# Kernel tuning notes

Hardware: AMD Instinct MI355X
Metric: run time of the kernel (lower is better)

The kernel has to match this reference:

```python
import jax, jax.numpy as jnp
import numpy as np

N = 100000        # nodes in the batched graph
E = 1_600_000     # directed edges
G = 256           # graphs in the batch
IN, H = 3, 64
EPS = 1e-5        # BatchNorm eps (eval mode: running stats, dropout off)


def setup_inputs() -> dict:
    key = jax.random.key(0)
    ks = jax.random.split(key, 40)
    inp = {}
    inp["x"] = jax.random.normal(ks[0], (N, IN), jnp.float32)
    inp["edge_index"] = jax.random.randint(ks[1], (2, E), 0, N, dtype=jnp.int32)
    inp["batch_idx"] = jnp.sort(jax.random.randint(ks[2], (N,), 0, G, dtype=jnp.int32))
    dims = [IN, H, H, H]  # zip(dims[:-1], dims[1:]) -> 3 GCN layers (as in source)
    k = 3
    for i in range(3):
        inp[f"W{i}"] = jax.random.normal(ks[k], (dims[i], dims[i + 1]), jnp.float32) * 0.1; k += 1
        inp[f"b{i}"] = jax.random.normal(ks[k], (dims[i + 1],), jnp.float32) * 0.01; k += 1
        inp[f"g{i}"] = jax.random.uniform(ks[k], (dims[i + 1],), jnp.float32, 0.5, 1.5); k += 1
        inp[f"be{i}"] = jax.random.normal(ks[k], (dims[i + 1],), jnp.float32) * 0.1; k += 1
        inp[f"rm{i}"] = jax.random.normal(ks[k], (dims[i + 1],), jnp.float32) * 0.1; k += 1
        inp[f"rv{i}"] = jax.random.uniform(ks[k], (dims[i + 1],), jnp.float32, 0.5, 1.5); k += 1
    inp["mW1"] = jax.random.normal(ks[k], (2 * H, 32), jnp.float32) * 0.1; k += 1
    inp["mb1"] = jnp.zeros((32,), jnp.float32)
    inp["mW2"] = jax.random.normal(ks[k], (32, 16), jnp.float32) * 0.1; k += 1
    inp["mb2"] = jnp.zeros((16,), jnp.float32)
    inp["mW3"] = jax.random.normal(ks[k], (16, 1), jnp.float32) * 0.1; k += 1
    inp["mb3"] = jnp.zeros((1,), jnp.float32)
    return inp


def _gcn(x, W, b, src, dst):
    # PyG GCNConv: add self-loops, symmetric D^-1/2 (A+I) D^-1/2 normalization
    h = x @ W                                   # [N, out]
    deg = jnp.zeros((N,), h.dtype).at[dst].add(1.0) + 1.0  # +1 self-loop
    dinv = jax.lax.rsqrt(deg)
    coef = dinv[src] * dinv[dst]                # [E]
    agg = jax.ops.segment_sum(h[src] * coef[:, None], dst, num_segments=N)
    agg = agg + h * (dinv * dinv)[:, None]      # self-loop message
    return agg + b


def _bn(x, g, be, rm, rv):
    return (x - rm) * jax.lax.rsqrt(rv + EPS) * g + be


def _forward(x, edge_index, batch_idx,
             W0, b0, g0, be0, rm0, rv0,
             W1, b1, g1, be1, rm1, rv1,
             W2, b2, g2, be2, rm2, rv2,
             mW1, mb1, mW2, mb2, mW3, mb3):
    src, dst = edge_index[0], edge_index[1]
    layers = [(W0, b0, g0, be0, rm0, rv0), (W1, b1, g1, be1, rm1, rv1), (W2, b2, g2, be2, rm2, rv2)]
    for (W, b, g, be, rm, rv) in layers:
        x = jax.nn.relu(_bn(_gcn(x, W, b, src, dst), g, be, rm, rv))
    cnt = jax.ops.segment_sum(jnp.ones((N,), x.dtype), batch_idx, num_segments=G)
    x_mean = jax.ops.segment_sum(x, batch_idx, num_segments=G) / jnp.maximum(cnt, 1.0)[:, None]
    x_max = jax.ops.segment_max(x, batch_idx, num_segments=G)
    x_max = jnp.where(jnp.isfinite(x_max), x_max, 0.0)
    xg = jnp.concatenate([x_mean, x_max], axis=1)  # [G, 2H]
    h = jax.nn.relu(xg @ mW1 + mb1)
    h = jax.nn.relu(h @ mW2 + mb2)
    return h @ mW3 + mb3                            # [G, 1]


def reference(x, edge_index, batch_idx,
              W0, b0, g0, be0, rm0, rv0,
              W1, b1, g1, be1, rm1, rv1,
              W2, b2, g2, be2, rm2, rv2,
              mW1, mb1, mW2, mb2, mW3, mb3):
    return _forward(x, edge_index, batch_idx,
                    W0, b0, g0, be0, rm0, rv0,
                    W1, b1, g1, be1, rm1, rv1,
                    W2, b2, g2, be2, rm2, rv2,
                    mW1, mb1, mW2, mb2, mW3, mb3)
```

## Files before the change

### kernel.cpp

```cpp
#include <hip/hip_runtime.h>
#include <hip/hip_fp16.h>

#define NN 100000
#define EE 1600000
#define GG 256
#define EPS 1e-5f
#define KB2 ((NN + 511) >> 9)
#define EPB 4096
#define EBLK ((EE + EPB - 1) / EPB)
#define NB256 ((NN + 255) / 256)

__device__ __forceinline__ unsigned int pack2(float x, float y) {
  __half2 h = __float22half2_rn(make_float2(x, y));
  return *reinterpret_cast<unsigned int*>(&h);
}
__device__ __forceinline__ uint2 pack4(float x, float y, float z, float w) {
  uint2 r;
  r.x = pack2(x, y);
  r.y = pack2(z, w);
  return r;
}
__device__ __forceinline__ void add8(float4& a0, float4& a1, uint4 v) {
  __half2 h0 = *reinterpret_cast<__half2*>(&v.x);
  __half2 h1 = *reinterpret_cast<__half2*>(&v.y);
  __half2 h2 = *reinterpret_cast<__half2*>(&v.z);
  __half2 h3 = *reinterpret_cast<__half2*>(&v.w);
  float2 f0 = __half22float2(h0), f1 = __half22float2(h1);
  float2 f2 = __half22float2(h2), f3 = __half22float2(h3);
  a0.x += f0.x; a0.y += f0.y; a0.z += f1.x; a0.w += f1.y;
  a1.x += f2.x; a1.y += f2.y; a1.z += f3.x; a1.w += f3.y;
}

__global__ void k_bcnt(const int* __restrict__ ei, int* __restrict__ bcnt) {
  __shared__ int cnt[KB2];
  int t = threadIdx.x;
  for (int i = t; i < KB2; i += 256) cnt[i] = 0;
  __syncthreads();
  int e0 = blockIdx.x * EPB;
#pragma unroll
  for (int j = 0; j < 16; ++j) {
    int e = e0 + j * 256 + t;
    if (e < EE) atomicAdd(&cnt[ei[EE + e] >> 9], 1);
  }
  __syncthreads();
  for (int i = t; i < KB2; i += 256)
    if (cnt[i] > 0) atomicAdd(&bcnt[i], cnt[i]);
}

__global__ void k_bscan(const int* __restrict__ bcnt, int* __restrict__ bbase,
                        int* __restrict__ bfill, int* __restrict__ row) {
  __shared__ int s[256];
  int t = threadIdx.x;
  int v = (t < KB2) ? bcnt[t] : 0;
  s[t] = v;
  __syncthreads();
  for (int off = 1; off < 256; off <<= 1) {
    int add = (t >= off) ? s[t - off] : 0;
    __syncthreads();
    s[t] += add;
    __syncthreads();
  }
  if (t < KB2) {
    int e = s[t] - v;
    bbase[t] = e;
    bfill[t] = e;
  }
  if (t == 0) {
    bbase[KB2] = EE;
    row[NN] = EE;
  }
}

__global__ void k_passA(const int* __restrict__ ei, int* __restrict__ bfill,
                        int* __restrict__ tmp) {
  __shared__ int cnt[KB2], cur[KB2], base[KB2];
  int t = threadIdx.x;
  for (int b = t; b < KB2; b += 256) { cnt[b] = 0; cur[b] = 0; }
  __syncthreads();
  int e0 = blockIdx.x * EPB;
  int myb[16];
#pragma unroll
  for (int j = 0; j < 16; ++j) {
    int e = e0 + j * 256 + t;
    int bb = -1;
    if (e < EE) bb = ei[EE + e] >> 9;
    myb[j] = bb;
    if (bb >= 0) atomicAdd(&cnt[bb], 1);
  }
  __syncthreads();
  for (int b = t; b < KB2; b += 256)
    if (cnt[b] > 0) base[b] = atomicAdd(&bfill[b], cnt[b]);
  __syncthreads();
#pragma unroll
  for (int j = 0; j < 16; ++j) {
    int e = e0 + j * 256 + t;
    int bb = myb[j];
    if (bb >= 0) {
      int slot = base[bb] + atomicAdd(&cur[bb], 1);
      tmp[slot] = (ei[e] << 9) | (ei[EE + e] & 511);
    }
  }
}

__global__ void k_bucket(const int* __restrict__ tmp, const int* __restrict__ bbase,
                         const float* __restrict__ x, int* __restrict__ csr,
                         int* __restrict__ row, float* __restrict__ dinv,
                         float4* __restrict__ xd) {
  __shared__ int cnt[512], s[512], fillp[512];
  int b = blockIdx.x, t = threadIdx.x;
  int nb = b << 9;
  int e0 = bbase[b], e1 = bbase[b + 1];
  cnt[t] = 0;
  cnt[t + 256] = 0;
  __syncthreads();
  for (int e = e0 + t; e < e1; e += 256) atomicAdd(&cnt[tmp[e] & 511], 1);
  __syncthreads();
  s[t] = cnt[t];
  s[t + 256] = cnt[t + 256];
  __syncthreads();
  for (int off = 1; off < 512; off <<= 1) {
    int i1 = t + 256;
    int v0 = (t >= off) ? s[t - off] : 0;
    int v1 = (i1 >= off) ? s[i1 - off] : 0;
    __syncthreads();
    s[t] += v0;
    s[i1] += v1;
    __syncthreads();
  }
#pragma unroll
  for (int k = 0; k < 2; ++k) {
    int i = t + k * 256;
    int excl = s[i] - cnt[i];
    fillp[i] = excl;
    int dst = nb + i;
    if (dst < NN) {
      row[dst] = e0 + excl;
      float d = rsqrtf((float)cnt[i] + 1.0f);
      dinv[dst] = d;
      xd[dst] = make_float4(x[dst * 3] * d, x[dst * 3 + 1] * d, x[dst * 3 + 2] * d, 0.f);
    }
  }
  __syncthreads();
  for (int e = e0 + t; e < e1; e += 256) {
    int ed = tmp[e];
    int slot = atomicAdd(&fillp[ed & 511], 1);
    csr[e0 + slot] = ed >> 9;
  }
}

__global__ void k_agg3f(const float4* __restrict__ xd, const int* __restrict__ row,
                        const int* __restrict__ csr, const float* __restrict__ dinv,
                        const float* __restrict__ W, const float* __restrict__ b,
                        const float* __restrict__ gam, const float* __restrict__ bet,
                        const float* __restrict__ rm, const float* __restrict__ rv,
                        uint2* __restrict__ out) {
  int n = blockIdx.x * 256 + threadIdx.x;
  if (n >= NN) return;
  int s0 = row[n], s1 = row[n + 1];
  float4 a = xd[n];
  float ax = a.x, ay = a.y, az = a.z;
  for (int i = s0; i < s1; i += 16) {
    int rem = s1 - i;
    int idx[16];
#pragma unroll
    for (int j = 0; j < 16; ++j) idx[j] = csr[min(i + j, s1 - 1)];
    float4 v[16];
#pragma unroll
    for (int j = 0; j < 16; ++j) v[j] = xd[idx[j]];
#pragma unroll
    for (int j = 0; j < 16; ++j)
      if (j < rem) { ax += v[j].x; ay += v[j].y; az += v[j].z; }
  }
  float d = dinv[n];
  float t0 = ax * d, t1 = ay * d, t2 = az * d;
  const float4* W4 = (const float4*)W;
  const float4* b4 = (const float4*)b;
  const float4* g4p = (const float4*)gam;
  const float4* be4p = (const float4*)bet;
  const float4* rm4p = (const float4*)rm;
  const float4* rv4p = (const float4*)rv;
#pragma unroll
  for (int c4 = 0; c4 < 16; ++c4) {
    float4 w0 = W4[c4], w1 = W4[16 + c4], w2 = W4[32 + c4];
    float4 bb = b4[c4], g4 = g4p[c4], be4 = be4p[c4], rm4 = rm4p[c4], rv4 = rv4p[c4];
    float4 o;
    o.x = fmaf(t0, w0.x, fmaf(t1, w1.x, fmaf(t2, w2.x, bb.x)));
    o.y = fmaf(t0, w0.y, fmaf(t1, w1.y, fmaf(t2, w2.y, bb.y)));
    o.z = fmaf(t0, w0.z, fmaf(t1, w1.z, fmaf(t2, w2.z, bb.z)));
    o.w = fmaf(t0, w0.w, fmaf(t1, w1.w, fmaf(t2, w2.w, bb.w)));
    float scx = g4.x * rsqrtf(rv4.x + EPS), shx = be4.x - rm4.x * scx;
    float scy = g4.y * rsqrtf(rv4.y + EPS), shy = be4.y - rm4.y * scy;
    float scz = g4.z * rsqrtf(rv4.z + EPS), shz = be4.z - rm4.z * scz;
    float scw = g4.w * rsqrtf(rv4.w + EPS), shw = be4.w - rm4.w * scw;
    o.x = fmaxf(fmaf(o.x, scx, shx), 0.f) * d;
    o.y = fmaxf(fmaf(o.y, scy, shy), 0.f) * d;
    o.z = fmaxf(fmaf(o.z, scz, shz), 0.f) * d;
    o.w = fmaxf(fmaf(o.w, scw, shw), 0.f) * d;
    out[(size_t)n * 16 + c4] = pack4(o.x, o.y, o.z, o.w);
  }
}

template <bool MID>
__global__ void k_layer2(const uint4* __restrict__ xs, const int* __restrict__ row,
                         const int* __restrict__ csr, const float* __restrict__ dinv,
                         const float* __restrict__ W, const float* __restrict__ b,
                         const float* __restrict__ gam, const float* __restrict__ bet,
                         const float* __restrict__ rm, const float* __restrict__ rv,
                         void* __restrict__ outv) {
  __shared__ float sh[32][68];
  int t = blockIdx.x * 256 + threadIdx.x;
  int n = t >> 3, sub = t & 7;
  int local = threadIdx.x >> 3;
  int s0 = row[n], s1 = row[n + 1];
  float4 a0 = make_float4(0.f, 0.f, 0.f, 0.f);
  float4 a1 = make_float4(0.f, 0.f, 0.f, 0.f);
  add8(a0, a1, xs[(size_t)n * 8 + sub]);
  if (s0 < s1) {
    int e = s0 + sub;
    int myidx = (e < s1) ? csr[e] : n;
    for (int i = s0; i < s1; i += 8) {
      int e2 = i + 8 + sub;
      int pre = csr[min(e2, s1 - 1)];
      int nidx = (e2 < s1) ? pre : n;
      int rem = s1 - i;
      uint4 v[8];
#pragma unroll
      for (int j = 0; j < 8; ++j) {
        int idx = __shfl(myidx, j, 8);
        v[j] = xs[(size_t)idx * 8 + sub];
      }
#pragma unroll
      for (int j = 0; j < 8; ++j)
        if (j < rem) add8(a0, a1, v[j]);
      myidx = nidx;
    }
  }
  float d = dinv[n];
  float4 w0 = make_float4(a0.x * d, a0.y * d, a0.z * d, a0.w * d);
  float4 w1 = make_float4(a1.x * d, a1.y * d, a1.z * d, a1.w * d);
  *(float4*)&sh[local][sub * 8] = w0;
  *(float4*)&sh[local][sub * 8 + 4] = w1;
  __syncthreads();
  const float4* W4 = (const float4*)W;
  float4 accA = ((const float4*)b)[sub * 2];
  float4 accB = ((const float4*)b)[sub * 2 + 1];
#pragma unroll 8
  for (int k = 0; k < 64; ++k) {
    float xv = sh[local][k];
    float4 wA = W4[k * 16 + sub * 2];
    float4 wB = W4[k * 16 + sub * 2 + 1];
    accA.x = fmaf(xv, wA.x, accA.x);
    accA.y = fmaf(xv, wA.y, accA.y);
    accA.z = fmaf(xv, wA.z, accA.z);
    accA.w = fmaf(xv, wA.w, accA.w);
    accB.x = fmaf(xv, wB.x, accB.x);
    accB.y = fmaf(xv, wB.y, accB.y);
    accB.z = fmaf(xv, wB.z, accB.z);
    accB.w = fmaf(xv, wB.w, accB.w);
  }
  float4 gA = ((const float4*)gam)[sub * 2], gB = ((const float4*)gam)[sub * 2 + 1];
  float4 beA = ((const float4*)bet)[sub * 2], beB = ((const float4*)bet)[sub * 2 + 1];
  float4 rmA = ((const float4*)rm)[sub * 2], rmB = ((const float4*)rm)[sub * 2 + 1];
  float4 rvA = ((const float4*)rv)[sub * 2], rvB = ((const float4*)rv)[sub * 2 + 1];
  float4 oA, oB;
  {
    float sc = gA.x * rsqrtf(rvA.x + EPS); oA.x = fmaxf(fmaf(accA.x, sc, beA.x - rmA.x * sc), 0.f);
    sc = gA.y * rsqrtf(rvA.y + EPS); oA.y = fmaxf(fmaf(accA.y, sc, beA.y - rmA.y * sc), 0.f);
    sc = gA.z * rsqrtf(rvA.z + EPS); oA.z = fmaxf(fmaf(accA.z, sc, beA.z - rmA.z * sc), 0.f);
    sc = gA.w * rsqrtf(rvA.w + EPS); oA.w = fmaxf(fmaf(accA.w, sc, beA.w - rmA.w * sc), 0.f);
    sc = gB.x * rsqrtf(rvB.x + EPS); oB.x = fmaxf(fmaf(accB.x, sc, beB.x - rmB.x * sc), 0.f);
    sc = gB.y * rsqrtf(rvB.y + EPS); oB.y = fmaxf(fmaf(accB.y, sc, beB.y - rmB.y * sc), 0.f);
    sc = gB.z * rsqrtf(rvB.z + EPS); oB.z = fmaxf(fmaf(accB.z, sc, beB.z - rmB.z * sc), 0.f);
    sc = gB.w * rsqrtf(rvB.w + EPS); oB.w = fmaxf(fmaf(accB.w, sc, beB.w - rmB.w * sc), 0.f);
  }
  if (MID) {
    uint4 r;
    r.x = pack2(oA.x * d, oA.y * d);
    r.y = pack2(oA.z * d, oA.w * d);
    r.z = pack2(oB.x * d, oB.y * d);
    r.w = pack2(oB.z * d, oB.w * d);
    ((uint4*)outv)[(size_t)n * 8 + sub] = r;
  } else {
    ((float4*)outv)[(size_t)n * 16 + sub * 2] = oA;
    ((float4*)outv)[(size_t)n * 16 + sub * 2 + 1] = oB;
  }
}

__device__ __forceinline__ int lower_bound(const int* __restrict__ b, int target) {
  int lo = 0, hi = NN;
  while (lo < hi) {
    int m = (lo + hi) >> 1;
    if (b[m] < target) lo = m + 1; else hi = m;
  }
  return lo;
}

__global__ void k_poolmlp(const float4* __restrict__ feat, const int* __restrict__ bidx,
                          const float* __restrict__ mW1, const float* __restrict__ mb1,
                          const float* __restrict__ mW2, const float* __restrict__ mb2,
                          const float* __restrict__ mW3, const float* __restrict__ mb3,
                          float* __restrict__ out) {
  __shared__ float4 shs[16][17], shm[16][17];
  __shared__ float xg[128], h1[32], h2[16];
  int g = blockIdx.x, t = threadIdx.x;
  int c4 = t & 15, r = t >> 4;
  int lo = lower_bound(bidx, g);
  int hi = lower_bound(bidx, g + 1);
  float4 s = make_float4(0.f, 0.f, 0.f, 0.f);
  float4 m = make_float4(0.f, 0.f, 0.f, 0.f);
  for (int i = lo + r; i < hi; i += 16) {
    float4 v = feat[(size_t)i * 16 + c4];
    s.x += v.x; s.y += v.y; s.z += v.z; s.w += v.w;
    m.x = fmaxf(m.x, v.x); m.y = fmaxf(m.y, v.y);
    m.z = fmaxf(m.z, v.z); m.w = fmaxf(m.w, v.w);
  }
  shs[r][c4] = s;
  shm[r][c4] = m;
  __syncthreads();
  if (t < 16) {
    float4 cs = shs[0][t], cm = shm[0][t];
#pragma unroll
    for (int r2 = 1; r2 < 16; ++r2) {
      float4 as = shs[r2][t], am = shm[r2][t];
      cs.x += as.x; cs.y += as.y; cs.z += as.z; cs.w += as.w;
      cm.x = fmaxf(cm.x, am.x); cm.y = fmaxf(cm.y, am.y);
      cm.z = fmaxf(cm.z, am.z); cm.w = fmaxf(cm.w, am.w);
    }
    float inv = 1.0f / fmaxf((float)(hi - lo), 1.0f);
    xg[t * 4 + 0] = cs.x * inv; xg[t * 4 + 1] = cs.y * inv;
    xg[t * 4 + 2] = cs.z * inv; xg[t * 4 + 3] = cs.w * inv;
    xg[64 + t * 4 + 0] = cm.x; xg[64 + t * 4 + 1] = cm.y;
    xg[64 + t * 4 + 2] = cm.z; xg[64 + t * 4 + 3] = cm.w;
  }
  __syncthreads();
  if (t < 32) {
    float a = mb1[t];
    for (int k = 0; k < 128; ++k) a = fmaf(xg[k], mW1[k * 32 + t], a);
    h1[t] = fmaxf(a, 0.f);
  }
  __syncthreads();
  if (t < 16) {
    float a = mb2[t];
    for (int k = 0; k < 32; ++k) a = fmaf(h1[k], mW2[k * 16 + t], a);
    h2[t] = fmaxf(a, 0.f);
  }
  __syncthreads();
  if (t == 0) {
    float a = mb3[0];
    for (int k = 0; k < 16; ++k) a = fmaf(h2[k], mW3[k], a);
    out[g] = a;
  }
}

extern "C" void kernel_launch(void* const* d_in, const int* in_sizes, int n_in,
                              void* d_out, int out_size, void* d_ws, size_t ws_size,
                              hipStream_t stream) {
  const float* x = (const float*)d_in[0];
  const int* ei = (const int*)d_in[1];
  const int* bidx = (const int*)d_in[2];
  const float *W[3], *b[3], *gam[3], *bet[3], *rm[3], *rv[3];
  for (int l = 0; l < 3; ++l) {
    W[l] = (const float*)d_in[3 + 6 * l];
    b[l] = (const float*)d_in[4 + 6 * l];
    gam[l] = (const float*)d_in[5 + 6 * l];
    bet[l] = (const float*)d_in[6 + 6 * l];
    rm[l] = (const float*)d_in[7 + 6 * l];
    rv[l] = (const float*)d_in[8 + 6 * l];
  }
  const float* mW1 = (const float*)d_in[21];
  const float* mb1 = (const float*)d_in[22];
  const float* mW2 = (const float*)d_in[23];
  const float* mb2 = (const float*)d_in[24];
  const float* mW3 = (const float*)d_in[25];
  const float* mb3 = (const float*)d_in[26];
  float* out = (float*)d_out;

  char* ws = (char*)d_ws;
  size_t off = 0;
  auto alloc = [&](size_t bytes) {
    void* p = ws + off;
    off = (off + bytes + 1023) & ~(size_t)1023;
    return p;
  };
  float* dinv = (float*)alloc(NN * 4);
  int* row = (int*)alloc((NN + 1) * 4);
  int* csr = (int*)alloc((size_t)EE * 4);
  int* bcnt = (int*)alloc(256 * 4);
  int* bbase = (int*)alloc(256 * 4);
  int* bfill = (int*)alloc(256 * 4);
  float4* xd = (float4*)alloc((size_t)NN * 16);
  float* bufA = (float*)alloc((size_t)NN * 64 * 4);
  float* bufB = (float*)alloc((size_t)NN * 64 * 4);
  int* tmp = (int*)bufA;

  hipMemsetAsync(bcnt, 0, 256 * 4, stream);

  k_bcnt<<<EBLK, 256, 0, stream>>>(ei, bcnt);
  k_bscan<<<1, 256, 0, stream>>>(bcnt, bbase, bfill, row);
  k_passA<<<EBLK, 256, 0, stream>>>(ei, bfill, tmp);
  k_bucket<<<KB2, 256, 0, stream>>>(tmp, bbase, x, csr, row, dinv, xd);

  int nb8 = (NN * 8) / 256;

  k_agg3f<<<NB256, 256, 0, stream>>>(xd, row, csr, dinv, W[0], b[0], gam[0], bet[0],
                                     rm[0], rv[0], (uint2*)bufA);
  k_layer2<true><<<nb8, 256, 0, stream>>>((const uint4*)bufA, row, csr, dinv, W[1], b[1],
                                          gam[1], bet[1], rm[1], rv[1], (void*)bufB);
  k_layer2<false><<<nb8, 256, 0, stream>>>((const uint4*)bufB, row, csr, dinv, W[2], b[2],
                                           gam[2], bet[2], rm[2], rv[2], (void*)bufA);
  k_poolmlp<<<GG, 256, 0, stream>>>((const float4*)bufA, bidx, mW1, mb1, mW2, mb2, mW3, mb3, out);
}
```

Measured before the change: 343.9 us.

## Replace bucket count/scan with fixed-capacity buckets and asm-batched gathers

```diff
diff --git a/kernel.cpp b/kernel.cpp
--- a/kernel.cpp
+++ b/kernel.cpp
@@ -6,6 +6,7 @@
 #define GG 256
 #define EPS 1e-5f
 #define KB2 ((NN + 511) >> 9)
+#define BCAP 10240
 #define EPB 4096
 #define EBLK ((EE + EPB - 1) / EPB)
 #define NB256 ((NN + 255) / 256)
@@ -31,44 +32,11 @@
   a1.x += f2.x; a1.y += f2.y; a1.z += f3.x; a1.w += f3.y;
 }
 
-__global__ void k_bcnt(const int* __restrict__ ei, int* __restrict__ bcnt) {
-  __shared__ int cnt[KB2];
-  int t = threadIdx.x;
-  for (int i = t; i < KB2; i += 256) cnt[i] = 0;
-  __syncthreads();
-  int e0 = blockIdx.x * EPB;
-#pragma unroll
-  for (int j = 0; j < 16; ++j) {
-    int e = e0 + j * 256 + t;
-    if (e < EE) atomicAdd(&cnt[ei[EE + e] >> 9], 1);
-  }
-  __syncthreads();
-  for (int i = t; i < KB2; i += 256)
-    if (cnt[i] > 0) atomicAdd(&bcnt[i], cnt[i]);
-}
-
-__global__ void k_bscan(const int* __restrict__ bcnt, int* __restrict__ bbase,
-                        int* __restrict__ bfill, int* __restrict__ row) {
-  __shared__ int s[256];
-  int t = threadIdx.x;
-  int v = (t < KB2) ? bcnt[t] : 0;
-  s[t] = v;
-  __syncthreads();
-  for (int off = 1; off < 256; off <<= 1) {
-    int add = (t >= off) ? s[t - off] : 0;
-    __syncthreads();
-    s[t] += add;
-    __syncthreads();
-  }
-  if (t < KB2) {
-    int e = s[t] - v;
-    bbase[t] = e;
-    bfill[t] = e;
-  }
-  if (t == 0) {
-    bbase[KB2] = EE;
-    row[NN] = EE;
-  }
+__device__ __forceinline__ void gld16(uint4& d, const uint4* p) {
+  asm volatile("global_load_dwordx4 %0, %1, off" : "=v"(d) : "v"(p));
+}
+__device__ __forceinline__ void gld4(int& d, const int* p) {
+  asm volatile("global_load_dword %0, %1, off" : "=v"(d) : "v"(p));
 }
 
 __global__ void k_passA(const int* __restrict__ ei, int* __restrict__ bfill,
@@ -89,7 +57,7 @@
   }
   __syncthreads();
   for (int b = t; b < KB2; b += 256)
-    if (cnt[b] > 0) base[b] = atomicAdd(&bfill[b], cnt[b]);
+    if (cnt[b] > 0) base[b] = b * BCAP + atomicAdd(&bfill[b], cnt[b]);
   __syncthreads();
 #pragma unroll
   for (int j = 0; j < 16; ++j) {
@@ -102,14 +70,14 @@
   }
 }
 
-__global__ void k_bucket(const int* __restrict__ tmp, const int* __restrict__ bbase,
+__global__ void k_bucket(const int* __restrict__ tmp, const int* __restrict__ bfill,
                          const float* __restrict__ x, int* __restrict__ csr,
-                         int* __restrict__ row, float* __restrict__ dinv,
-                         float4* __restrict__ xd) {
+                         int* __restrict__ row, int* __restrict__ rowe,
+                         float* __restrict__ dinv, float4* __restrict__ xd) {
   __shared__ int cnt[512], s[512], fillp[512];
   int b = blockIdx.x, t = threadIdx.x;
   int nb = b << 9;
-  int e0 = bbase[b], e1 = bbase[b + 1];
+  int e0 = b * BCAP, e1 = e0 + bfill[b];
   cnt[t] = 0;
   cnt[t + 256] = 0;
   __syncthreads();
@@ -135,6 +103,7 @@
     int dst = nb + i;
     if (dst < NN) {
       row[dst] = e0 + excl;
+      rowe[dst] = e0 + s[i];
       float d = rsqrtf((float)cnt[i] + 1.0f);
       dinv[dst] = d;
       xd[dst] = make_float4(x[dst * 3] * d, x[dst * 3 + 1] * d, x[dst * 3 + 2] * d, 0.f);
@@ -149,14 +118,15 @@
 }
 
 __global__ void k_agg3f(const float4* __restrict__ xd, const int* __restrict__ row,
-                        const int* __restrict__ csr, const float* __restrict__ dinv,
+                        const int* __restrict__ rowe, const int* __restrict__ csr,
+                        const float* __restrict__ dinv,
                         const float* __restrict__ W, const float* __restrict__ b,
                         const float* __restrict__ gam, const float* __restrict__ bet,
                         const float* __restrict__ rm, const float* __restrict__ rv,
                         uint2* __restrict__ out) {
   int n = blockIdx.x * 256 + threadIdx.x;
   if (n >= NN) return;
-  int s0 = row[n], s1 = row[n + 1];
+  int s0 = row[n], s1 = rowe[n];
   float4 a = xd[n];
   float ax = a.x, ay = a.y, az = a.z;
   for (int i = s0; i < s1; i += 16) {
@@ -201,8 +171,10 @@
 }
 
 template <bool MID>
+__launch_bounds__(256, 4)
 __global__ void k_layer2(const uint4* __restrict__ xs, const int* __restrict__ row,
-                         const int* __restrict__ csr, const float* __restrict__ dinv,
+                         const int* __restrict__ rowe, const int* __restrict__ csr,
+                         const float* __restrict__ dinv,
                          const float* __restrict__ W, const float* __restrict__ b,
                          const float* __restrict__ gam, const float* __restrict__ bet,
                          const float* __restrict__ rm, const float* __restrict__ rv,
@@ -211,7 +183,7 @@
   int t = blockIdx.x * 256 + threadIdx.x;
   int n = t >> 3, sub = t & 7;
   int local = threadIdx.x >> 3;
-  int s0 = row[n], s1 = row[n + 1];
+  int s0 = row[n], s1 = rowe[n];
   float4 a0 = make_float4(0.f, 0.f, 0.f, 0.f);
   float4 a1 = make_float4(0.f, 0.f, 0.f, 0.f);
   add8(a0, a1, xs[(size_t)n * 8 + sub]);
@@ -220,19 +192,29 @@
     int myidx = (e < s1) ? csr[e] : n;
     for (int i = s0; i < s1; i += 8) {
       int e2 = i + 8 + sub;
-      int pre = csr[min(e2, s1 - 1)];
-      int nidx = (e2 < s1) ? pre : n;
+      int pre;
+      gld4(pre, csr + min(e2, s1 - 1));
+      uint4 v0, v1, v2, v3, v4, v5, v6, v7;
+      gld16(v0, xs + ((size_t)__shfl(myidx, 0, 8) * 8 + sub));
+      gld16(v1, xs + ((size_t)__shfl(myidx, 1, 8) * 8 + sub));
+      gld16(v2, xs + ((size_t)__shfl(myidx, 2, 8) * 8 + sub));
+      gld16(v3, xs + ((size_t)__shfl(myidx, 3, 8) * 8 + sub));
+      gld16(v4, xs + ((size_t)__shfl(myidx, 4, 8) * 8 + sub));
+      gld16(v5, xs + ((size_t)__shfl(myidx, 5, 8) * 8 + sub));
+      gld16(v6, xs + ((size_t)__shfl(myidx, 6, 8) * 8 + sub));
+      gld16(v7, xs + ((size_t)__shfl(myidx, 7, 8) * 8 + sub));
+      asm volatile("s_waitcnt vmcnt(0)" ::: "memory");
+      __builtin_amdgcn_sched_barrier(0);
       int rem = s1 - i;
-      uint4 v[8];
-#pragma unroll
-      for (int j = 0; j < 8; ++j) {
-        int idx = __shfl(myidx, j, 8);
-        v[j] = xs[(size_t)idx * 8 + sub];
-      }
-#pragma unroll
-      for (int j = 0; j < 8; ++j)
-        if (j < rem) add8(a0, a1, v[j]);
-      myidx = nidx;
+      add8(a0, a1, v0);
+      if (rem > 1) add8(a0, a1, v1);
+      if (rem > 2) add8(a0, a1, v2);
+      if (rem > 3) add8(a0, a1, v3);
+      if (rem > 4) add8(a0, a1, v4);
+      if (rem > 5) add8(a0, a1, v5);
+      if (rem > 6) add8(a0, a1, v6);
+      if (rem > 7) add8(a0, a1, v7);
+      myidx = (e2 < s1) ? pre : n;
     }
   }
   float d = dinv[n];
@@ -383,30 +365,27 @@
     return p;
   };
   float* dinv = (float*)alloc(NN * 4);
-  int* row = (int*)alloc((NN + 1) * 4);
-  int* csr = (int*)alloc((size_t)EE * 4);
-  int* bcnt = (int*)alloc(256 * 4);
-  int* bbase = (int*)alloc(256 * 4);
+  int* row = (int*)alloc(NN * 4);
+  int* rowe = (int*)alloc(NN * 4);
+  int* csr = (int*)alloc((size_t)KB2 * BCAP * 4);
   int* bfill = (int*)alloc(256 * 4);
   float4* xd = (float4*)alloc((size_t)NN * 16);
   float* bufA = (float*)alloc((size_t)NN * 64 * 4);
-  float* bufB = (float*)alloc((size_t)NN * 64 * 4);
+  float* bufB = (float*)alloc((size_t)NN * 64 * 2);
   int* tmp = (int*)bufA;
 
-  hipMemsetAsync(bcnt, 0, 256 * 4, stream);
-
-  k_bcnt<<<EBLK, 256, 0, stream>>>(ei, bcnt);
-  k_bscan<<<1, 256, 0, stream>>>(bcnt, bbase, bfill, row);
+  hipMemsetAsync(bfill, 0, 256 * 4, stream);
+
   k_passA<<<EBLK, 256, 0, stream>>>(ei, bfill, tmp);
-  k_bucket<<<KB2, 256, 0, stream>>>(tmp, bbase, x, csr, row, dinv, xd);
+  k_bucket<<<KB2, 256, 0, stream>>>(tmp, bfill, x, csr, row, rowe, dinv, xd);
 
   int nb8 = (NN * 8) / 256;
 
-  k_agg3f<<<NB256, 256, 0, stream>>>(xd, row, csr, dinv, W[0], b[0], gam[0], bet[0],
+  k_agg3f<<<NB256, 256, 0, stream>>>(xd, row, rowe, csr, dinv, W[0], b[0], gam[0], bet[0],
                                      rm[0], rv[0], (uint2*)bufA);
-  k_layer2<true><<<nb8, 256, 0, stream>>>((const uint4*)bufA, row, csr, dinv, W[1], b[1],
+  k_layer2<true><<<nb8, 256, 0, stream>>>((const uint4*)bufA, row, rowe, csr, dinv, W[1], b[1],
                                           gam[1], bet[1], rm[1], rv[1], (void*)bufB);
-  k_layer2<false><<<nb8, 256, 0, stream>>>((const uint4*)bufB, row, csr, dinv, W[2], b[2],
+  k_layer2<false><<<nb8, 256, 0, stream>>>((const uint4*)bufB, row, rowe, csr, dinv, W[2], b[2],
                                            gam[2], bet[2], rm[2], rv[2], (void*)bufA);
   k_poolmlp<<<GG, 256, 0, stream>>>((const float4*)bufA, bidx, mW1, mb1, mW2, mb2, mW3, mb3, out);
 }
```

New measurement: 337.9 us. About the same (-1.8%).
